# Kernel tuning notes

Hardware: AMD Instinct MI355X
Metric: run time of the kernel (lower is better)

The kernel has to match this reference:

```python
import jax, jax.numpy as jnp
import numpy as np

# ---- problem constants (mirrors ScalarBorn defaults: accuracy=4, pml_width=20) ----
NY, NX = 200, 200
PML = 20
FD_PAD = 2            # accuracy // 2
PAD = PML + FD_PAD    # total halo on each side
DY = DX = 4.0         # grid_spacing
DT = 5e-4             # dt (stable: v_max*DT/DX ~ 0.31)
PML_FREQ = 25.0
NT = 120
N_SHOTS, N_SRC, N_REC = 2, 1, 100

# 4th-order central FD coefficients for offsets [-2,-1,0,1,2]
_D1 = [1.0/12.0, -2.0/3.0, 0.0, 2.0/3.0, -1.0/12.0]
_D2 = [-1.0/12.0, 4.0/3.0, -5.0/2.0, 4.0/3.0, -1.0/12.0]


def _deriv(w, coeffs, axis, scale):
    n = w.shape[axis]
    pad = [(0, 0)] * w.ndim
    pad[axis] = (FD_PAD, FD_PAD)
    wp = jnp.pad(w, pad)  # zero (Dirichlet) beyond padded domain
    out = None
    for i, c in enumerate(coeffs):
        if c == 0.0:
            continue
        t = c * jax.lax.slice_in_dim(wp, i, i + n, axis=axis)
        out = t if out is None else out + t
    return out * scale


def d1y(w): return _deriv(w, _D1, 1, 1.0 / DY)
def d1x(w): return _deriv(w, _D1, 2, 1.0 / DX)
def d2y(w): return _deriv(w, _D2, 1, 1.0 / (DY * DY))
def d2x(w): return _deriv(w, _D2, 2, 1.0 / (DX * DX))


def _pml_profile(n, h, max_vel):
    """CPML decay (a) and input (b) coefficients along one axis of the padded grid."""
    x = jnp.arange(n, dtype=jnp.float32)
    lo = FD_PAD + PML
    hi = n - 1 - FD_PAD - PML
    d = jnp.maximum(jnp.clip((lo - x) / PML, 0.0, 1.0),
                    jnp.clip((x - hi) / PML, 0.0, 1.0))  # normalized depth into PML
    sigma = 3.0 * max_vel * np.log(1000.0) / (2.0 * PML * h) * d ** 2
    alpha = 2.0 * np.pi * PML_FREQ * (1.0 - d)
    a = jnp.exp(-(sigma + alpha) * DT)
    b = sigma / (sigma + alpha + 1e-9) * (a - 1.0)  # b == 0 in interior (sigma == 0)
    return a, b


def setup_inputs() -> dict:
    key = jax.random.key(0)
    k1, k2, k3, k4, k5, k6 = jax.random.split(key, 6)
    v = 1500.0 + 1000.0 * jax.random.uniform(k1, (NY, NX), jnp.float32)
    scatter = 100.0 * jax.random.normal(k2, (NY, NX), jnp.float32)
    source_amplitudes = jax.random.normal(k3, (N_SHOTS, N_SRC, NT), jnp.float32)
    sy = jax.random.randint(k4, (N_SHOTS, N_SRC), 10, NY - 10)
    sx = jax.random.randint(k5, (N_SHOTS, N_SRC), 10, NX - 10)
    source_locations = jnp.stack([sy, sx], -1).astype(jnp.int32)
    ry = jax.random.randint(k6, (N_SHOTS, N_REC), 10, NY - 10)
    rx = jax.random.randint(jax.random.fold_in(k6, 1), (N_SHOTS, N_REC), 10, NX - 10)
    receiver_locations = jnp.stack([ry, rx], -1).astype(jnp.int32)
    return {"v": v, "scatter": scatter, "source_amplitudes": source_amplitudes,
            "source_locations": source_locations, "receiver_locations": receiver_locations}


def reference(v, scatter, source_amplitudes, source_locations, receiver_locations):
    """Scalar Born propagation: background + scattered wavefields with CPML.
    Returns receiver_amplitudes [shot, receiver, time] recorded from the
    scattered wavefield (the primary output of scalar_born)."""
    nyp, nxp = NY + 2 * PAD, NX + 2 * PAD
    vp = jnp.pad(v, PAD, mode="edge")          # replicate model into halo
    sp = jnp.pad(scatter, PAD)                  # zero scattering in PML
    max_vel = jax.lax.stop_gradient(jnp.max(vp))
    ay1, by1 = _pml_profile(nyp, DY, max_vel)
    ax1, bx1 = _pml_profile(nxp, DX, max_vel)
    ay, by = ay1[None, :, None], by1[None, :, None]
    ax, bx = ax1[None, None, :], bx1[None, None, :]
    v2dt2 = vp ** 2 * (DT ** 2)

    sl = source_locations.astype(jnp.int32) + PAD      # (B, n_src, 2)
    rl = receiver_locations.astype(jnp.int32) + PAD    # (B, n_rec, 2)
    bidx = jnp.arange(N_SHOTS)[:, None]
    src_scale = v2dt2[sl[..., 0], sl[..., 1]]          # (B, n_src)

    z = jnp.zeros((N_SHOTS, nyp, nxp), v.dtype)
    carry0 = (z,) * 12
    amps = jnp.moveaxis(source_amplitudes, -1, 0)      # (nt, B, n_src)

    def spatial(w, psiy, psix, zetay, zetax):
        # CPML-augmented Laplacian: d2w + d(psi) + zeta per axis
        psiy_n = ay * psiy + by * d1y(w)
        psix_n = ax * psix + bx * d1x(w)
        ty = d2y(w) + d1y(psiy_n)
        tx = d2x(w) + d1x(psix_n)
        zetay_n = ay * zetay + by * ty
        zetax_n = ax * zetax + bx * tx
        return ty + zetay_n + tx + zetax_n, psiy_n, psix_n, zetay_n, zetax_n

    def step(carry, amp_t):
        (wfc, wfp, psiy, psix, zetay, zetax,
         wfcsc, wfpsc, psiysc, psixsc, zetaysc, zetaxsc) = carry
        lap, psiy, psix, zetay, zetax = spatial(wfc, psiy, psix, zetay, zetax)
        lapsc, psiysc, psixsc, zetaysc, zetaxsc = spatial(wfcsc, psiysc, psixsc, zetaysc, zetaxsc)
        wfn = v2dt2 * lap + 2.0 * wfc - wfp
        # Born coupling: scattered field driven by 2*v*dt^2*scatter * L[wfc]
        wfnsc = v2dt2 * lapsc + 2.0 * wfcsc - wfpsc + 2.0 * vp * (DT ** 2) * sp * lap
        wfn = wfn.at[bidx, sl[..., 0], sl[..., 1]].add(src_scale * amp_t)
        rec = wfnsc[bidx, rl[..., 0], rl[..., 1]]      # (B, n_rec)
        new_carry = (wfn, wfc, psiy, psix, zetay, zetax,
                     wfnsc, wfcsc, psiysc, psixsc, zetaysc, zetaxsc)
        return new_carry, rec

    _, recs = jax.lax.scan(step, carry0, amps)
    return jnp.moveaxis(recs, 0, -1)  # (B, n_rec, nt)
```

## Files before the change

### kernel.cpp

```cpp
#include <hip/hip_runtime.h>

#define NYI 200
#define NXI 200
#define PMLW 20
#define FDP 2
#define PADW (PMLW + FDP)
#define NYP (NYI + 2 * PADW)
#define NXP (NXI + 2 * PADW)
#define NP  (NYP * NXP)
#define NSH 2
#define NRECV 100
#define NTT 120
#define TOTC (NSH * NP)

#define DTC   0.0005f
#define RH    0.25f
#define RH2   0.0625f
#define C1A   (1.0f / 12.0f)
#define C1B   (2.0f / 3.0f)
#define C2A   (1.0f / 12.0f)
#define C2B   (4.0f / 3.0f)

#define PML_LO 22
#define PML_HI 221

#define KST   4
#define HALO  (4 * KST)
#define OUTY  32
#define OUTX  16
#define SY    (OUTY + 2 * HALO)
#define SX    (OUTX + 2 * HALO)
#define QX    (SX / 4)
#define NQ    (SY * QX)
#define NQP   776
#define TBT   NQ
#define TILESY 8
#define TILESX 16
#define NBLK  (TILESY * TILESX * NSH)

typedef float f4 __attribute__((ext_vector_type(4)));

#define OFF_MAXV 0
#define OFF_AY   64
#define OFF_BY   (OFF_AY + NYP)
#define OFF_AX   (OFF_BY + NYP)
#define OFF_BX   (OFF_AX + NXP)
#define OFF_V2   (OFF_BX + NXP)
#define OFF_SPV  (OFF_V2 + NP)
#define OFF_F    (OFF_SPV + NP)

#define LD4(p) (*reinterpret_cast<const f4*>(p))
#define ST4(p, vv) (*reinterpret_cast<f4*>(p) = (vv))

__global__ void reduce_max_kernel(const float* __restrict__ v, float* __restrict__ out) {
    int i = blockIdx.x * 256 + threadIdx.x;
    float m = 0.0f;
    for (; i < NYI * NXI; i += gridDim.x * 256)
        m = fmaxf(m, v[i]);
    #pragma unroll
    for (int o = 32; o > 0; o >>= 1)
        m = fmaxf(m, __shfl_down(m, o));
    if ((threadIdx.x & 63) == 0)
        atomicMax((int*)out, __float_as_int(m));
}

__global__ void setup_kernel(const float* __restrict__ v,
                             const float* __restrict__ scat,
                             const float* __restrict__ maxv,
                             float* __restrict__ ay, float* __restrict__ by,
                             float* __restrict__ ax, float* __restrict__ bx,
                             float* __restrict__ v2dt2, float* __restrict__ spv) {
    int gtid = blockIdx.x * blockDim.x + threadIdx.x;
    int nth  = gridDim.x * blockDim.x;

    for (int idx = gtid; idx < NP; idx += nth) {
        int y = idx / NXP;
        int x = idx - y * NXP;
        int yi = min(max(y - PADW, 0), NYI - 1);
        int xi = min(max(x - PADW, 0), NXI - 1);
        float vp = v[yi * NXI + xi];
        v2dt2[idx] = vp * vp * DTC * DTC;
        float sp = 0.0f;
        int ys = y - PADW, xs = x - PADW;
        if (ys >= 0 && ys < NYI && xs >= 0 && xs < NXI)
            sp = scat[ys * NXI + xs];
        spv[idx] = 2.0f * vp * DTC * DTC * sp;
    }

    if (gtid < NYP + NXP) {
        float mv = maxv[0];
        int isY = gtid < NYP;
        int j   = isY ? gtid : gtid - NYP;
        int n   = isY ? NYP : NXP;
        float h = 4.0f;
        float xf = (float)j;
        float lo = (float)(FDP + PMLW);
        float hi = (float)(n - 1 - FDP - PMLW);
        float d1 = fminf(fmaxf((lo - xf) / (float)PMLW, 0.0f), 1.0f);
        float d2 = fminf(fmaxf((xf - hi) / (float)PMLW, 0.0f), 1.0f);
        float d  = fmaxf(d1, d2);
        float sigma = 3.0f * mv * 6.9077552790f / (2.0f * (float)PMLW * h) * d * d;
        float alpha = 6.2831853072f * 25.0f * (1.0f - d);
        float a  = expf(-(sigma + alpha) * DTC);
        float bb = sigma / (sigma + alpha + 1e-9f) * (a - 1.0f);
        if (isY) { ay[j] = a; by[j] = bb; }
        else     { ax[j] = a; bx[j] = bb; }
    }
}

__device__ __forceinline__ void xshift(const f4 L, const f4 C, const f4 R,
                                       f4& m2, f4& m1, f4& p1, f4& p2) {
    m2 = (f4){L.z, L.w, C.x, C.y};
    m1 = (f4){L.w, C.x, C.y, C.z};
    p1 = (f4){C.y, C.z, C.w, R.x};
    p2 = (f4){C.z, C.w, R.x, R.y};
}

__global__ __launch_bounds__(TBT)
void tstep_kernel(int t0,
    const float* __restrict__ Gin, float* __restrict__ Gout,
    const float* __restrict__ v2g, const float* __restrict__ spg,
    const float* __restrict__ ayg, const float* __restrict__ byg,
    const float* __restrict__ axg, const float* __restrict__ bxg,
    const float* __restrict__ amps, const int* __restrict__ sloc,
    const int* __restrict__ rloc, float* __restrict__ out)
{
    __shared__ f4 sW[2][NQP];
    __shared__ f4 sPy[2][NQP];
    __shared__ f4 sPx[2][NQP];

    const int tid  = threadIdx.x;
    const int bid  = blockIdx.x;
    const int tyid = bid & 7;
    const int jj   = bid >> 3;
    const int txid = jj & 15;
    const int shot = jj >> 4;
    const int oy = tyid * OUTY - HALO;
    const int ox = txid * OUTX - HALO;
    const int fb = shot * NP;

    const int ly  = tid / QX;
    const int qx  = tid - ly * QX;
    const int lx0 = 4 * qx;
    const int gy  = oy + ly;
    const int gx0 = ox + lx0;
    const bool iby = (unsigned)gy  < (unsigned)NYP;
    const bool ibx = (unsigned)gx0 < (unsigned)NXP;
    const bool ib  = iby && ibx;
    const int g = ib ? (fb + gy * NXP + gx0) : 0;

    const bool pY = ib && (gy < PML_LO || gy > PML_HI);
    const bool pX = ib && (gx0 < PML_LO || gx0 + 3 > PML_HI);

    const f4 z4 = {0.f, 0.f, 0.f, 0.f};

    f4 wC[2], wP[2], py[2], px[2], zy[2], zx[2];
    wC[0] = ib ? LD4(Gin + 0 * TOTC + g) : z4;
    wC[1] = ib ? LD4(Gin + 6 * TOTC + g) : z4;
    sW[0][tid] = wC[0];
    sW[1][tid] = wC[1];
    py[0] = pY ? LD4(Gin + 2 * TOTC + g) : z4;
    py[1] = pY ? LD4(Gin + 8 * TOTC + g) : z4;
    px[0] = pX ? LD4(Gin + 3 * TOTC + g) : z4;
    px[1] = pX ? LD4(Gin + 9 * TOTC + g) : z4;
    sPy[0][tid] = py[0];
    sPy[1][tid] = py[1];
    sPx[0][tid] = px[0];
    sPx[1][tid] = px[1];

    wP[0] = ib ? LD4(Gin + 1  * TOTC + g) : z4;
    wP[1] = ib ? LD4(Gin + 7  * TOTC + g) : z4;
    zy[0] = pY ? LD4(Gin + 4  * TOTC + g) : z4;
    zy[1] = pY ? LD4(Gin + 10 * TOTC + g) : z4;
    zx[0] = pX ? LD4(Gin + 5  * TOTC + g) : z4;
    zx[1] = pX ? LD4(Gin + 11 * TOTC + g) : z4;

    const float ayv = ib ? ayg[gy] : 0.f;
    const float byv = ib ? byg[gy] : 0.f;
    f4 axq = z4, bxq = z4, v2v = z4, spvv = z4;
    if (ib) {
        axq  = LD4(axg + gx0);
        bxq  = LD4(bxg + gx0);
        v2v  = LD4(v2g + gy * NXP + gx0);
        spvv = LD4(spg + gy * NXP + gx0);
    }
    f4 srcv = z4;
    {
        const int sy  = sloc[shot * 2 + 0] + PADW;
        const int sxx = sloc[shot * 2 + 1] + PADW;
        #pragma unroll
        for (int c = 0; c < 4; ++c)
            if (ib && gy == sy && gx0 + c == sxx) srcv[c] = v2v[c];
    }

    const int my = min(ly, SY - 1 - ly);
    int mxmax = 0;
    #pragma unroll
    for (int c = 0; c < 4; ++c)
        mxmax = max(mxmax, min(lx0 + c, SX - 1 - (lx0 + c)));
    const int mq = min(my, mxmax);

    const int qiL = tid - (qx > 0 ? 1 : 0);
    const int qiR = tid + (qx < QX - 1 ? 1 : 0);

    float ampv[KST];
    #pragma unroll
    for (int s = 0; s < KST; ++s) ampv[s] = amps[shot * NTT + t0 + s];

    bool recOwn = false; int rq = 0, rc = 0, rout = 0;
    float recv[KST];
    if (tid < NSH * NRECV) {
        int rb = tid / NRECV;
        int ry = rloc[tid * 2 + 0] + PADW;
        int rx = rloc[tid * 2 + 1] + PADW;
        if (rb == shot && ry / OUTY == tyid && rx / OUTX == txid) {
            recOwn = true;
            int lry = ry - oy, lrx = rx - ox;
            rq = lry * QX + (lrx >> 2);
            rc = lrx & 3;
            rout = tid * NTT;
        }
    }
    __syncthreads();

    #pragma unroll
    for (int s = 0; s < KST; ++s) {
        const int mA = 4 * s + 2;
        const int mB = 4 * s + 4;
        f4 d2ys[2], d2xs[2];

        if (mq >= mA) {
            #pragma unroll
            for (int f = 0; f < 2; ++f) {
                f4 m2 = sW[f][tid - 2 * QX];
                f4 m1 = sW[f][tid - QX];
                f4 p1 = sW[f][tid + QX];
                f4 p2 = sW[f][tid + 2 * QX];
                f4 L  = sW[f][qiL];
                f4 R  = sW[f][qiR];
                f4 xm2, xm1, xp1, xp2;
                xshift(L, wC[f], R, xm2, xm1, xp1, xp2);
                f4 d1y = RH * (C1A * (m2 - p2) + C1B * (p1 - m1));
                f4 d1x = RH * (C1A * (xm2 - xp2) + C1B * (xp1 - xm1));
                d2ys[f] = RH2 * (C2B * (m1 + p1) - C2A * (m2 + p2) - 2.5f * wC[f]);
                d2xs[f] = RH2 * (C2B * (xm1 + xp1) - C2A * (xm2 + xp2) - 2.5f * wC[f]);
                py[f] = ayv * py[f] + byv * d1y;
                px[f] = axq * px[f] + bxq * d1x;
                sPy[f][tid] = py[f];
                sPx[f][tid] = px[f];
            }
        }
        __syncthreads();

        if (mq >= mB) {
            f4 lap0 = z4;
            #pragma unroll
            for (int f = 0; f < 2; ++f) {
                f4 pym2 = sPy[f][tid - 2 * QX], pym1 = sPy[f][tid - QX];
                f4 pyp1 = sPy[f][tid + QX],     pyp2 = sPy[f][tid + 2 * QX];
                f4 d1yp = RH * (C1A * (pym2 - pyp2) + C1B * (pyp1 - pym1));

                f4 pL = sPx[f][qiL], pR = sPx[f][qiR];
                f4 qm2, qm1, qp1, qp2;
                xshift(pL, px[f], pR, qm2, qm1, qp1, qp2);
                f4 d1xp = RH * (C1A * (qm2 - qp2) + C1B * (qp1 - qm1));

                f4 ty = d2ys[f] + d1yp;
                f4 tx = d2xs[f] + d1xp;
                zy[f] = ayv * zy[f] + byv * ty;
                zx[f] = axq * zx[f] + bxq * tx;
                f4 lap = ty + zy[f] + tx + zx[f];

                f4 wn;
                if (f == 0) {
                    lap0 = lap;
                    wn = v2v * lap + 2.0f * wC[0] - wP[0] + srcv * ampv[s];
                } else {
                    wn = v2v * lap + 2.0f * wC[1] - wP[1] + spvv * lap0;
                }
                wP[f] = wC[f];
                wC[f] = wn;
                sW[f][tid] = wn;
            }
        }
        __syncthreads();

        if (recOwn) recv[s] = sW[1][rq][rc];
    }

    if (recOwn) {
        #pragma unroll
        for (int s = 0; s < KST; ++s)
            out[rout + t0 + s] = recv[s];
    }

    const bool outq = ib && (unsigned)(ly - HALO) < (unsigned)OUTY
                         && (unsigned)(lx0 - HALO) < (unsigned)OUTX;
    if (outq) {
        ST4(Gout + 0 * TOTC + g, wC[0]);
        ST4(Gout + 1 * TOTC + g, wP[0]);
        ST4(Gout + 6 * TOTC + g, wC[1]);
        ST4(Gout + 7 * TOTC + g, wP[1]);
        if (pY) {
            ST4(Gout + 2  * TOTC + g, py[0]);
            ST4(Gout + 4  * TOTC + g, zy[0]);
            ST4(Gout + 8  * TOTC + g, py[1]);
            ST4(Gout + 10 * TOTC + g, zy[1]);
        }
        if (pX) {
            ST4(Gout + 3  * TOTC + g, px[0]);
            ST4(Gout + 5  * TOTC + g, zx[0]);
            ST4(Gout + 9  * TOTC + g, px[1]);
            ST4(Gout + 11 * TOTC + g, zx[1]);
        }
    }
}

extern "C" void kernel_launch(void* const* d_in, const int* in_sizes, int n_in,
                              void* d_out, int out_size, void* d_ws, size_t ws_size,
                              hipStream_t stream) {
    const float* v    = (const float*)d_in[0];
    const float* scat = (const float*)d_in[1];
    const float* amps = (const float*)d_in[2];
    const int* sloc = (const int*)d_in[3];
    const int* rloc = (const int*)d_in[4];
    float* ws = (float*)d_ws;
    float* out = (float*)d_out;

    float* ay  = ws + OFF_AY;
    float* by  = ws + OFF_BY;
    float* ax  = ws + OFF_AX;
    float* bx  = ws + OFF_BX;
    float* v2  = ws + OFF_V2;
    float* spv = ws + OFF_SPV;
    float* bank0 = ws + OFF_F;
    float* bank1 = bank0 + 12 * TOTC;

    hipMemsetAsync(bank0, 0, sizeof(float) * 12 * TOTC, stream);

    reduce_max_kernel<<<64, 256, 0, stream>>>(v, ws + OFF_MAXV);
    setup_kernel<<<(NP + 255) / 256, 256, 0, stream>>>(
        v, scat, ws + OFF_MAXV, ay, by, ax, bx, v2, spv);

    float* gin  = bank0;
    float* gout = bank1;
    for (int t0 = 0; t0 < NTT; t0 += KST) {
        tstep_kernel<<<NBLK, TBT, 0, stream>>>(
            t0, gin, gout, v2, spv, ay, by, ax, bx, amps, sloc, rloc, out);
        float* tmp = gin; gin = gout; gout = tmp;
    }
}
```

Baseline: 411.4 us.

## Compute two rows per thread to reuse vertical stencil loads from LDS

Each thread now owns two vertically adjacent quad-cells instead of one, halving the block size. Neighbouring rows share the y-stencil reads, cutting LDS traffic per output point. Loads of wP and the zeta/psi state are also skipped for halo cells that never reach the update threshold. The cost is higher register pressure, fewer threads per block, and more divergent masking.

```diff
diff --git a/kernel.cpp b/kernel.cpp
--- a/kernel.cpp
+++ b/kernel.cpp
@@ -32,8 +32,8 @@
 #define SX    (OUTX + 2 * HALO)
 #define QX    (SX / 4)
 #define NQ    (SY * QX)
-#define NQP   776
-#define TBT   NQ
+#define NQP   860
+#define TBT   (NQ / 2)
 #define TILESY 8
 #define TILESX 16
 #define NBLK  (TILESY * TILESX * NSH)
@@ -139,69 +139,88 @@
     const int ox = txid * OUTX - HALO;
     const int fb = shot * NP;
 
-    const int ly  = tid / QX;
-    const int qx  = tid - ly * QX;
+    const int rp  = tid / QX;
+    const int qx  = tid - rp * QX;
+    const int r0  = 2 * rp;
     const int lx0 = 4 * qx;
-    const int gy  = oy + ly;
+    const int gy0 = oy + r0, gy1 = gy0 + 1;
     const int gx0 = ox + lx0;
-    const bool iby = (unsigned)gy  < (unsigned)NYP;
     const bool ibx = (unsigned)gx0 < (unsigned)NXP;
-    const bool ib  = iby && ibx;
-    const int g = ib ? (fb + gy * NXP + gx0) : 0;
-
-    const bool pY = ib && (gy < PML_LO || gy > PML_HI);
-    const bool pX = ib && (gx0 < PML_LO || gx0 + 3 > PML_HI);
+    const bool ib0 = ibx && (unsigned)gy0 < (unsigned)NYP;
+    const bool ib1 = ibx && (unsigned)gy1 < (unsigned)NYP;
+    const int g0 = ib0 ? (fb + gy0 * NXP + gx0) : 0;
+    const int g1 = ib1 ? (fb + gy1 * NXP + gx0) : 0;
+
+    const bool pY0 = ib0 && (gy0 < PML_LO || gy0 > PML_HI);
+    const bool pY1 = ib1 && (gy1 < PML_LO || gy1 > PML_HI);
+    const bool pX  = ibx && (gx0 < PML_LO || gx0 + 3 > PML_HI);
+
+    const int mx = min(lx0 + 3, SX - 1 - lx0);
+    const int m0 = min(min(r0, SY - 1 - r0), mx);
+    const int m1 = min(min(r0 + 1, SY - 2 - r0), mx);
+    const int mmax = max(m0, m1);
+
+    const int i0  = r0 * QX + qx, i1 = i0 + QX;
+    const int im2 = max(r0 - 2, 0) * QX + qx;
+    const int im1 = max(r0 - 1, 0) * QX + qx;
+    const int ip2 = min(r0 + 2, SY - 1) * QX + qx;
+    const int ip3 = min(r0 + 3, SY - 1) * QX + qx;
+    const int oL = (qx > 0) ? 1 : 0, oR = (qx < QX - 1) ? 1 : 0;
+    const int iL0 = i0 - oL, iR0 = i0 + oR, iL1 = i1 - oL, iR1 = i1 + oR;
 
     const f4 z4 = {0.f, 0.f, 0.f, 0.f};
 
-    f4 wC[2], wP[2], py[2], px[2], zy[2], zx[2];
-    wC[0] = ib ? LD4(Gin + 0 * TOTC + g) : z4;
-    wC[1] = ib ? LD4(Gin + 6 * TOTC + g) : z4;
-    sW[0][tid] = wC[0];
-    sW[1][tid] = wC[1];
-    py[0] = pY ? LD4(Gin + 2 * TOTC + g) : z4;
-    py[1] = pY ? LD4(Gin + 8 * TOTC + g) : z4;
-    px[0] = pX ? LD4(Gin + 3 * TOTC + g) : z4;
-    px[1] = pX ? LD4(Gin + 9 * TOTC + g) : z4;
-    sPy[0][tid] = py[0];
-    sPy[1][tid] = py[1];
-    sPx[0][tid] = px[0];
-    sPx[1][tid] = px[1];
-
-    wP[0] = ib ? LD4(Gin + 1  * TOTC + g) : z4;
-    wP[1] = ib ? LD4(Gin + 7  * TOTC + g) : z4;
-    zy[0] = pY ? LD4(Gin + 4  * TOTC + g) : z4;
-    zy[1] = pY ? LD4(Gin + 10 * TOTC + g) : z4;
-    zx[0] = pX ? LD4(Gin + 5  * TOTC + g) : z4;
-    zx[1] = pX ? LD4(Gin + 11 * TOTC + g) : z4;
-
-    const float ayv = ib ? ayg[gy] : 0.f;
-    const float byv = ib ? byg[gy] : 0.f;
-    f4 axq = z4, bxq = z4, v2v = z4, spvv = z4;
-    if (ib) {
-        axq  = LD4(axg + gx0);
-        bxq  = LD4(bxg + gx0);
-        v2v  = LD4(v2g + gy * NXP + gx0);
-        spvv = LD4(spg + gy * NXP + gx0);
-    }
-    f4 srcv = z4;
+    f4 wC[2][2], wP[2][2], py[2][2], px[2][2], zy[2][2], zx[2][2];
+    wC[0][0] = ib0 ? LD4(Gin + 0 * TOTC + g0) : z4;
+    wC[0][1] = ib1 ? LD4(Gin + 0 * TOTC + g1) : z4;
+    wC[1][0] = ib0 ? LD4(Gin + 6 * TOTC + g0) : z4;
+    wC[1][1] = ib1 ? LD4(Gin + 6 * TOTC + g1) : z4;
+    sW[0][i0] = wC[0][0];
+    sW[0][i1] = wC[0][1];
+    sW[1][i0] = wC[1][0];
+    sW[1][i1] = wC[1][1];
+
+    const bool ld0b = ib0 && m0 >= 4, ld1b = ib1 && m1 >= 4;
+    const bool ld0a = m0 >= 2, ld1a = m1 >= 2;
+    wP[0][0] = ld0b ? LD4(Gin + 1 * TOTC + g0) : z4;
+    wP[0][1] = ld1b ? LD4(Gin + 1 * TOTC + g1) : z4;
+    wP[1][0] = ld0b ? LD4(Gin + 7 * TOTC + g0) : z4;
+    wP[1][1] = ld1b ? LD4(Gin + 7 * TOTC + g1) : z4;
+    py[0][0] = (pY0 && ld0a) ? LD4(Gin + 2 * TOTC + g0) : z4;
+    py[0][1] = (pY1 && ld1a) ? LD4(Gin + 2 * TOTC + g1) : z4;
+    py[1][0] = (pY0 && ld0a) ? LD4(Gin + 8 * TOTC + g0) : z4;
+    py[1][1] = (pY1 && ld1a) ? LD4(Gin + 8 * TOTC + g1) : z4;
+    px[0][0] = (pX && ld0a) ? LD4(Gin + 3 * TOTC + g0) : z4;
+    px[0][1] = (pX && ld1a) ? LD4(Gin + 3 * TOTC + g1) : z4;
+    px[1][0] = (pX && ld0a) ? LD4(Gin + 9 * TOTC + g0) : z4;
+    px[1][1] = (pX && ld1a) ? LD4(Gin + 9 * TOTC + g1) : z4;
+    zy[0][0] = (pY0 && ld0b) ? LD4(Gin + 4 * TOTC + g0) : z4;
+    zy[0][1] = (pY1 && ld1b) ? LD4(Gin + 4 * TOTC + g1) : z4;
+    zy[1][0] = (pY0 && ld0b) ? LD4(Gin + 10 * TOTC + g0) : z4;
+    zy[1][1] = (pY1 && ld1b) ? LD4(Gin + 10 * TOTC + g1) : z4;
+    zx[0][0] = (pX && ld0b) ? LD4(Gin + 5 * TOTC + g0) : z4;
+    zx[0][1] = (pX && ld1b) ? LD4(Gin + 5 * TOTC + g1) : z4;
+    zx[1][0] = (pX && ld0b) ? LD4(Gin + 11 * TOTC + g0) : z4;
+    zx[1][1] = (pX && ld1b) ? LD4(Gin + 11 * TOTC + g1) : z4;
+
+    const float ay0 = ib0 ? ayg[gy0] : 0.f, by0 = ib0 ? byg[gy0] : 0.f;
+    const float ay1 = ib1 ? ayg[gy1] : 0.f, by1 = ib1 ? byg[gy1] : 0.f;
+    f4 axq = z4, bxq = z4;
+    f4 v2v0 = z4, v2v1 = z4, spv0 = z4, spv1 = z4;
+    if (ibx) { axq = LD4(axg + gx0); bxq = LD4(bxg + gx0); }
+    if (ib0) { v2v0 = LD4(v2g + gy0 * NXP + gx0); spv0 = LD4(spg + gy0 * NXP + gx0); }
+    if (ib1) { v2v1 = LD4(v2g + gy1 * NXP + gx0); spv1 = LD4(spg + gy1 * NXP + gx0); }
+
+    f4 srcv0 = z4, srcv1 = z4;
     {
         const int sy  = sloc[shot * 2 + 0] + PADW;
         const int sxx = sloc[shot * 2 + 1] + PADW;
         #pragma unroll
-        for (int c = 0; c < 4; ++c)
-            if (ib && gy == sy && gx0 + c == sxx) srcv[c] = v2v[c];
-    }
-
-    const int my = min(ly, SY - 1 - ly);
-    int mxmax = 0;
-    #pragma unroll
-    for (int c = 0; c < 4; ++c)
-        mxmax = max(mxmax, min(lx0 + c, SX - 1 - (lx0 + c)));
-    const int mq = min(my, mxmax);
-
-    const int qiL = tid - (qx > 0 ? 1 : 0);
-    const int qiR = tid + (qx < QX - 1 ? 1 : 0);
+        for (int c = 0; c < 4; ++c) {
+            if (ib0 && gy0 == sy && gx0 + c == sxx) srcv0[c] = v2v0[c];
+            if (ib1 && gy1 == sy && gx0 + c == sxx) srcv1[c] = v2v1[c];
+        }
+    }
 
     float ampv[KST];
     #pragma unroll
@@ -227,60 +246,94 @@
     for (int s = 0; s < KST; ++s) {
         const int mA = 4 * s + 2;
         const int mB = 4 * s + 4;
-        f4 d2ys[2], d2xs[2];
-
-        if (mq >= mA) {
+        f4 d2ys[2][2], d2xs[2][2];
+
+        if (mmax >= mA) {
             #pragma unroll
             for (int f = 0; f < 2; ++f) {
-                f4 m2 = sW[f][tid - 2 * QX];
-                f4 m1 = sW[f][tid - QX];
-                f4 p1 = sW[f][tid + QX];
-                f4 p2 = sW[f][tid + 2 * QX];
-                f4 L  = sW[f][qiL];
-                f4 R  = sW[f][qiR];
+                f4 ym1 = sW[f][im1], yp2 = sW[f][ip2];
+                f4 ym2 = sW[f][im2], yp3 = sW[f][ip3];
+                f4 L0 = sW[f][iL0], R0 = sW[f][iR0];
+                f4 L1 = sW[f][iL1], R1 = sW[f][iR1];
                 f4 xm2, xm1, xp1, xp2;
-                xshift(L, wC[f], R, xm2, xm1, xp1, xp2);
-                f4 d1y = RH * (C1A * (m2 - p2) + C1B * (p1 - m1));
-                f4 d1x = RH * (C1A * (xm2 - xp2) + C1B * (xp1 - xm1));
-                d2ys[f] = RH2 * (C2B * (m1 + p1) - C2A * (m2 + p2) - 2.5f * wC[f]);
-                d2xs[f] = RH2 * (C2B * (xm1 + xp1) - C2A * (xm2 + xp2) - 2.5f * wC[f]);
-                py[f] = ayv * py[f] + byv * d1y;
-                px[f] = axq * px[f] + bxq * d1x;
-                sPy[f][tid] = py[f];
-                sPx[f][tid] = px[f];
+
+                xshift(L0, wC[f][0], R0, xm2, xm1, xp1, xp2);
+                f4 d1y0 = RH * (C1A * (ym2 - yp2) + C1B * (wC[f][1] - ym1));
+                f4 d1x0 = RH * (C1A * (xm2 - xp2) + C1B * (xp1 - xm1));
+                d2ys[f][0] = RH2 * (C2B * (ym1 + wC[f][1]) - C2A * (ym2 + yp2) - 2.5f * wC[f][0]);
+                d2xs[f][0] = RH2 * (C2B * (xm1 + xp1) - C2A * (xm2 + xp2) - 2.5f * wC[f][0]);
+                if (m0 >= mA) {
+                    py[f][0] = ay0 * py[f][0] + by0 * d1y0;
+                    px[f][0] = axq * px[f][0] + bxq * d1x0;
+                    sPy[f][i0] = py[f][0];
+                    sPx[f][i0] = px[f][0];
+                }
+                xshift(L1, wC[f][1], R1, xm2, xm1, xp1, xp2);
+                f4 d1y1 = RH * (C1A * (ym1 - yp3) + C1B * (yp2 - wC[f][0]));
+                f4 d1x1 = RH * (C1A * (xm2 - xp2) + C1B * (xp1 - xm1));
+                d2ys[f][1] = RH2 * (C2B * (wC[f][0] + yp2) - C2A * (ym1 + yp3) - 2.5f * wC[f][1]);
+                d2xs[f][1] = RH2 * (C2B * (xm1 + xp1) - C2A * (xm2 + xp2) - 2.5f * wC[f][1]);
+                if (m1 >= mA) {
+                    py[f][1] = ay1 * py[f][1] + by1 * d1y1;
+                    px[f][1] = axq * px[f][1] + bxq * d1x1;
+                    sPy[f][i1] = py[f][1];
+                    sPx[f][i1] = px[f][1];
+                }
             }
         }
         __syncthreads();
 
-        if (mq >= mB) {
-            f4 lap0 = z4;
+        if (mmax >= mB) {
+            f4 lap0r0 = z4, lap0r1 = z4;
             #pragma unroll
             for (int f = 0; f < 2; ++f) {
-                f4 pym2 = sPy[f][tid - 2 * QX], pym1 = sPy[f][tid - QX];
-                f4 pyp1 = sPy[f][tid + QX],     pyp2 = sPy[f][tid + 2 * QX];
-                f4 d1yp = RH * (C1A * (pym2 - pyp2) + C1B * (pyp1 - pym1));
-
-                f4 pL = sPx[f][qiL], pR = sPx[f][qiR];
+                f4 pym1 = sPy[f][im1], pyp2 = sPy[f][ip2];
+                f4 pym2 = sPy[f][im2], pyp3 = sPy[f][ip3];
+                f4 pL0 = sPx[f][iL0], pR0 = sPx[f][iR0];
+                f4 pL1 = sPx[f][iL1], pR1 = sPx[f][iR1];
                 f4 qm2, qm1, qp1, qp2;
-                xshift(pL, px[f], pR, qm2, qm1, qp1, qp2);
-                f4 d1xp = RH * (C1A * (qm2 - qp2) + C1B * (qp1 - qm1));
-
-                f4 ty = d2ys[f] + d1yp;
-                f4 tx = d2xs[f] + d1xp;
-                zy[f] = ayv * zy[f] + byv * ty;
-                zx[f] = axq * zx[f] + bxq * tx;
-                f4 lap = ty + zy[f] + tx + zx[f];
-
-                f4 wn;
-                if (f == 0) {
-                    lap0 = lap;
-                    wn = v2v * lap + 2.0f * wC[0] - wP[0] + srcv * ampv[s];
-                } else {
-                    wn = v2v * lap + 2.0f * wC[1] - wP[1] + spvv * lap0;
+
+                f4 d1yp0 = RH * (C1A * (pym2 - pyp2) + C1B * (py[f][1] - pym1));
+                xshift(pL0, px[f][0], pR0, qm2, qm1, qp1, qp2);
+                f4 d1xp0 = RH * (C1A * (qm2 - qp2) + C1B * (qp1 - qm1));
+                f4 d1yp1 = RH * (C1A * (pym1 - pyp3) + C1B * (pyp2 - py[f][0]));
+                xshift(pL1, px[f][1], pR1, qm2, qm1, qp1, qp2);
+                f4 d1xp1 = RH * (C1A * (qm2 - qp2) + C1B * (qp1 - qm1));
+
+                if (m0 >= mB) {
+                    f4 tyv = d2ys[f][0] + d1yp0;
+                    f4 txv = d2xs[f][0] + d1xp0;
+                    zy[f][0] = ay0 * zy[f][0] + by0 * tyv;
+                    zx[f][0] = axq * zx[f][0] + bxq * txv;
+                    f4 lap = tyv + zy[f][0] + txv + zx[f][0];
+                    f4 wn;
+                    if (f == 0) {
+                        lap0r0 = lap;
+                        wn = v2v0 * lap + 2.0f * wC[0][0] - wP[0][0] + srcv0 * ampv[s];
+                    } else {
+                        wn = v2v0 * lap + 2.0f * wC[1][0] - wP[1][0] + spv0 * lap0r0;
+                    }
+                    wP[f][0] = wC[f][0];
+                    wC[f][0] = wn;
+                    sW[f][i0] = wn;
                 }
-                wP[f] = wC[f];
-                wC[f] = wn;
-                sW[f][tid] = wn;
+                if (m1 >= mB) {
+                    f4 tyv = d2ys[f][1] + d1yp1;
+                    f4 txv = d2xs[f][1] + d1xp1;
+                    zy[f][1] = ay1 * zy[f][1] + by1 * tyv;
+                    zx[f][1] = axq * zx[f][1] + bxq * txv;
+                    f4 lap = tyv + zy[f][1] + txv + zx[f][1];
+                    f4 wn;
+                    if (f == 0) {
+                        lap0r1 = lap;
+                        wn = v2v1 * lap + 2.0f * wC[0][1] - wP[0][1] + srcv1 * ampv[s];
+                    } else {
+                        wn = v2v1 * lap + 2.0f * wC[1][1] - wP[1][1] + spv1 * lap0r1;
+                    }
+                    wP[f][1] = wC[f][1];
+                    wC[f][1] = wn;
+                    sW[f][i1] = wn;
+                }
             }
         }
         __syncthreads();
@@ -294,24 +347,44 @@
             out[rout + t0 + s] = recv[s];
     }
 
-    const bool outq = ib && (unsigned)(ly - HALO) < (unsigned)OUTY
+    const bool oq0 = ib0 && (unsigned)(r0 - HALO) < (unsigned)OUTY
                          && (unsigned)(lx0 - HALO) < (unsigned)OUTX;
-    if (outq) {
-        ST4(Gout + 0 * TOTC + g, wC[0]);
-        ST4(Gout + 1 * TOTC + g, wP[0]);
-        ST4(Gout + 6 * TOTC + g, wC[1]);
-        ST4(Gout + 7 * TOTC + g, wP[1]);
-        if (pY) {
-            ST4(Gout + 2  * TOTC + g, py[0]);
-            ST4(Gout + 4  * TOTC + g, zy[0]);
-            ST4(Gout + 8  * TOTC + g, py[1]);
-            ST4(Gout + 10 * TOTC + g, zy[1]);
+    const bool oq1 = ib1 && (unsigned)(r0 + 1 - HALO) < (unsigned)OUTY
+                         && (unsigned)(lx0 - HALO) < (unsigned)OUTX;
+    if (oq0) {
+        ST4(Gout + 0 * TOTC + g0, wC[0][0]);
+        ST4(Gout + 1 * TOTC + g0, wP[0][0]);
+        ST4(Gout + 6 * TOTC + g0, wC[1][0]);
+        ST4(Gout + 7 * TOTC + g0, wP[1][0]);
+        if (pY0) {
+            ST4(Gout + 2  * TOTC + g0, py[0][0]);
+            ST4(Gout + 4  * TOTC + g0, zy[0][0]);
+            ST4(Gout + 8  * TOTC + g0, py[1][0]);
+            ST4(Gout + 10 * TOTC + g0, zy[1][0]);
         }
         if (pX) {
-            ST4(Gout + 3  * TOTC + g, px[0]);
-            ST4(Gout + 5  * TOTC + g, zx[0]);
-            ST4(Gout + 9  * TOTC + g, px[1]);
-            ST4(Gout + 11 * TOTC + g, zx[1]);
+            ST4(Gout + 3  * TOTC + g0, px[0][0]);
+            ST4(Gout + 5  * TOTC + g0, zx[0][0]);
+            ST4(Gout + 9  * TOTC + g0, px[1][0]);
+            ST4(Gout + 11 * TOTC + g0, zx[1][0]);
+        }
+    }
+    if (oq1) {
+        ST4(Gout + 0 * TOTC + g1, wC[0][1]);
+        ST4(Gout + 1 * TOTC + g1, wP[0][1]);
+        ST4(Gout + 6 * TOTC + g1, wC[1][1]);
+        ST4(Gout + 7 * TOTC + g1, wP[1][1]);
+        if (pY1) {
+            ST4(Gout + 2  * TOTC + g1, py[0][1]);
+            ST4(Gout + 4  * TOTC + g1, zy[0][1]);
+            ST4(Gout + 8  * TOTC + g1, py[1][1]);
+            ST4(Gout + 10 * TOTC + g1, zy[1][1]);
+        }
+        if (pX) {
+            ST4(Gout + 3  * TOTC + g1, px[0][1]);
+            ST4(Gout + 5  * TOTC + g1, zx[0][1]);
+            ST4(Gout + 9  * TOTC + g1, px[1][1]);
+            ST4(Gout + 11 * TOTC + g1, zx[1][1]);
         }
     }
 }
```

Result: slower. 1.530 ms (+272.0%).
